# Optimization experiments

Hardware: AMD Instinct MI355X
Metric: run time of the kernel (lower is better)

Reference implementation:

```python
import jax, jax.numpy as jnp
import numpy as np
import math

D_MODEL = 1024
N_HEADS = 16
D_K = D_MODEL // N_HEADS
THETA = 0.1


def setup_inputs() -> dict:
    key = jax.random.key(0)
    ks = jax.random.split(key, 6)
    scale = np.sqrt(1.0 / D_MODEL).astype(np.float32)
    x = jax.random.normal(ks[0], (4, 2048, D_MODEL), dtype=jnp.float32)
    W_q = jax.random.normal(ks[1], (D_MODEL, D_MODEL), dtype=jnp.float32) * scale
    W_k = jax.random.normal(ks[2], (D_MODEL, D_MODEL), dtype=jnp.float32) * scale
    W_v = jax.random.normal(ks[3], (D_MODEL, D_MODEL), dtype=jnp.float32) * scale
    W_o = jax.random.normal(ks[4], (D_MODEL, D_MODEL), dtype=jnp.float32) * scale
    alpha = jnp.ones((1,), dtype=jnp.float32)
    return {"x": x, "W_q": W_q, "W_k": W_k, "W_v": W_v, "W_o": W_o, "alpha": alpha}


def reference(x, W_q, W_k, W_v, W_o, alpha):
    B, S, _ = x.shape
    Q = x @ W_q
    K = x @ W_k
    V = x @ W_v
    # non-commutative elementwise transforms
    Q = Q + THETA * jnp.sin(Q)
    K = K + THETA * jnp.cos(K)
    V = V + alpha * THETA * jnp.tanh(V)
    # split heads: [B, H, S, d_k]
    def split(t):
        return t.reshape(B, S, N_HEADS, D_K).transpose(0, 2, 1, 3)
    Qh, Kh, Vh = split(Q), split(K), split(V)
    scores = jnp.einsum('bhqd,bhkd->bhqk', Qh, Kh) / math.sqrt(D_K)
    attn = jax.nn.softmax(scores, axis=-1)
    out = jnp.einsum('bhqk,bhkd->bhqd', attn, Vh)
    out = out.transpose(0, 2, 1, 3).reshape(B, S, D_MODEL)
    return out @ W_o
```

## Files before the change

kernel.cpp:

```cpp
#include <hip/hip_runtime.h>

typedef __bf16 bf16x8 __attribute__((ext_vector_type(8)));
typedef float f32x4 __attribute__((ext_vector_type(4)));
typedef float f32x16 __attribute__((ext_vector_type(16)));

#define MFMA16(a,b,c) __builtin_amdgcn_mfma_f32_16x16x32_bf16(a,b,c,0,0,0)
#define MFMA32(a,b,c) __builtin_amdgcn_mfma_f32_32x32x16_bf16(a,b,c,0,0,0)

__device__ __forceinline__ unsigned short f2bf(float f) {
  unsigned int u = __float_as_uint(f);
  u = (u + 0x7FFFu + ((u >> 16) & 1u)) >> 16;
  return (unsigned short)u;
}

__device__ __forceinline__ void gload16(const void* g, void* l) {
  __builtin_amdgcn_global_load_lds(
      (const __attribute__((address_space(1))) void*)g,
      (__attribute__((address_space(3))) void*)l, 16, 0, 0);
}

__device__ __forceinline__ float vexp2(float x) {
  float r;
  asm("v_exp_f32 %0, %1" : "=v"(r) : "v"(x));
  return r;
}

__device__ __forceinline__ bf16x8 mk_pfrag(int hi, float p0, float p1, float p2, float p3,
                                           float p4, float p5, float p6, float p7) {
  unsigned int a0, a1, b0, b1;
  asm("v_cvt_pk_bf16_f32 %0, %1, %2" : "=v"(a0) : "v"(p0), "v"(p1));
  asm("v_cvt_pk_bf16_f32 %0, %1, %2" : "=v"(a1) : "v"(p2), "v"(p3));
  asm("v_cvt_pk_bf16_f32 %0, %1, %2" : "=v"(b0) : "v"(p4), "v"(p5));
  asm("v_cvt_pk_bf16_f32 %0, %1, %2" : "=v"(b1) : "v"(p6), "v"(p7));
  unsigned int x = __shfl_xor(hi ? a0 : b0, 32);
  unsigned int y = __shfl_xor(hi ? a1 : b1, 32);
  uint4 w;
  w.x = hi ? x : a0;
  w.y = hi ? y : a1;
  w.z = hi ? b0 : x;
  w.w = hi ? b1 : y;
  return *reinterpret_cast<bf16x8*>(&w);
}

__global__ __launch_bounds__(256) void k_convx(const float* __restrict__ x,
                                               unsigned short* __restrict__ xb) {
  int i = (blockIdx.x * 256 + threadIdx.x) * 4;
  float4 v = *reinterpret_cast<const float4*>(x + i);
  ushort4 o;
  o.x = f2bf(v.x); o.y = f2bf(v.y); o.z = f2bf(v.z); o.w = f2bf(v.w);
  *reinterpret_cast<ushort4*>(xb + i) = o;
}

__global__ __launch_bounds__(256) void k_transw(const float* __restrict__ W,
                                                unsigned short* __restrict__ WT) {
  __shared__ float t[32][33];
  int bx = blockIdx.x * 32;
  int by = blockIdx.y * 32;
  int tx = threadIdx.x & 31;
  int ty = threadIdx.x >> 5;
#pragma unroll
  for (int i = 0; i < 32; i += 8)
    t[ty + i][tx] = W[(size_t)(by + ty + i) * 1024 + bx + tx];
  __syncthreads();
#pragma unroll
  for (int i = 0; i < 32; i += 8)
    WT[(size_t)(bx + ty + i) * 1024 + by + tx] = f2bf(t[tx][ty + i]);
}

template <int EPI>
__global__ __launch_bounds__(256) void k_gemm(
    const unsigned short* __restrict__ A, const unsigned short* __restrict__ BT, int K,
    unsigned short* __restrict__ Qf, unsigned short* __restrict__ Kf,
    unsigned short* __restrict__ VT, const float* __restrict__ alphaPtr,
    float* __restrict__ Out) {
  __shared__ __align__(16) unsigned short smem[128 * 136];
  unsigned short* AsBase = smem;
  unsigned short* BsBase = smem + 128 * 32;
  const int tid = threadIdx.x;
  const int wave = tid >> 6, lane = tid & 63;
  const int l15 = lane & 15, lg = lane >> 4;
  const int wr = wave >> 1, wc = wave & 1;
  const int bm = blockIdx.x, bn = blockIdx.y;

  f32x4 acc[4][4] = {};
  const unsigned short* Ab = A + (size_t)bm * 128 * K;
  const unsigned short* Bb = BT + (size_t)bn * 128 * K;

  const int r0 = tid >> 2, q0 = (tid & 3) * 8;
  const int r1 = r0 + 64;
  char* ldsA = (char*)AsBase + wave * 1024;
  char* ldsB = (char*)BsBase + wave * 1024;

  for (int k0 = 0; k0 < K; k0 += 32) {
    gload16((const void*)(Ab + (size_t)r0 * K + k0 + q0), ldsA);
    gload16((const void*)(Ab + (size_t)r1 * K + k0 + q0), ldsA + 4096);
    gload16((const void*)(Bb + (size_t)r0 * K + k0 + q0), ldsB);
    gload16((const void*)(Bb + (size_t)r1 * K + k0 + q0), ldsB + 4096);
    __syncthreads();
    bf16x8 af[4], bfr[4];
#pragma unroll
    for (int mi = 0; mi < 4; ++mi)
      af[mi] = *reinterpret_cast<const bf16x8*>(&AsBase[(wr * 64 + mi * 16 + l15) * 32 + lg * 8]);
#pragma unroll
    for (int ni = 0; ni < 4; ++ni)
      bfr[ni] = *reinterpret_cast<const bf16x8*>(&BsBase[(wc * 64 + ni * 16 + l15) * 32 + lg * 8]);
#pragma unroll
    for (int mi = 0; mi < 4; ++mi)
#pragma unroll
      for (int ni = 0; ni < 4; ++ni)
        acc[mi][ni] = MFMA16(af[mi], bfr[ni], acc[mi][ni]);
    __syncthreads();
  }

  if (EPI == 0) {
    const float av = alphaPtr[0];
    const int t = bn >> 3;
    if (t == 2) {
#pragma unroll
      for (int mi = 0; mi < 4; ++mi) {
        int row0 = bm * 128 + wr * 64 + mi * 16 + lg * 4;
        int bb = row0 >> 11, s = row0 & 2047;
#pragma unroll
        for (int ni = 0; ni < 4; ++ni) {
          int col = (bn & 7) * 128 + wc * 64 + ni * 16 + l15;
          int hh = col >> 6, dd = col & 63;
          ushort4 pk;
#pragma unroll
          for (int r = 0; r < 4; ++r) {
            float v = acc[mi][ni][r];
            float e = __expf(2.0f * v);
            v += av * 0.1f * (1.0f - 2.0f * __builtin_amdgcn_rcpf(e + 1.0f));
            ((unsigned short*)&pk)[r] = f2bf(v);
          }
          *reinterpret_cast<ushort4*>(VT + ((size_t)(bb * 16 + hh) * 64 + dd) * 2048 + s) = pk;
        }
      }
    } else {
#pragma unroll
      for (int mi = 0; mi < 4; ++mi)
#pragma unroll
        for (int ni = 0; ni < 4; ++ni)
#pragma unroll
          for (int r = 0; r < 4; ++r) {
            int row = wr * 64 + mi * 16 + lg * 4 + r;
            int col = wc * 64 + ni * 16 + l15;
            float v = acc[mi][ni][r];
            if (t == 0) {
              v += 0.1f * __sinf(v);
              v *= 0.18033688011112042f;
            } else {
              v += 0.1f * __cosf(v);
            }
            smem[row * 136 + col] = f2bf(v);
          }
      __syncthreads();
      unsigned short* dst = (t == 0) ? Qf : Kf;
      const int c16 = tid & 15, rb = tid >> 4;
      const int ncol0 = (bn & 7) * 128;
#pragma unroll
      for (int i2 = 0; i2 < 8; ++i2) {
        int srow = rb + i2 * 16;
        uint4 val = *reinterpret_cast<const uint4*>(&smem[srow * 136 + c16 * 8]);
        *reinterpret_cast<uint4*>(dst + (size_t)(bm * 128 + srow) * 1024 + ncol0 + c16 * 8) = val;
      }
    }
  } else {
#pragma unroll
    for (int ni = 0; ni < 4; ++ni) {
      int n = bn * 128 + wc * 64 + ni * 16 + l15;
#pragma unroll
      for (int mi = 0; mi < 4; ++mi) {
        int row = bm * 128 + wr * 64 + mi * 16 + lg * 4;
#pragma unroll
        for (int r = 0; r < 4; ++r)
          Out[(size_t)(row + r) * 1024 + n] = acc[mi][ni][r];
      }
    }
  }
}

__global__ __launch_bounds__(256)
__attribute__((amdgpu_waves_per_eu(4, 4)))
void k_attn(const unsigned short* __restrict__ Qf,
            const unsigned short* __restrict__ Kf,
            const unsigned short* __restrict__ VT,
            unsigned short* __restrict__ AO) {
  __shared__ __align__(16) unsigned short smem[3 * 8192];
  const int tid = threadIdx.x;
  const int wave = tid >> 6, lane = tid & 63;
  const int l31 = lane & 31, hi = lane >> 5;
  const int f = (blockIdx.y << 4) | blockIdx.x;
  const int nf = ((f & 7) << 7) | (f >> 3);
  const int qb = nf & 15, bh = nf >> 4;
  const int b = bh >> 4, h = bh & 15;

  const unsigned short* Qb = Qf + ((size_t)b * 2048 + qb * 128 + wave * 32) * 1024 + h * 64;
  const unsigned short* Kb = Kf + (size_t)b * 2048 * 1024 + h * 64;
  const unsigned short* Vb = VT + (size_t)bh * 64 * 2048;

  bf16x8 qfr[4];
#pragma unroll
  for (int ds = 0; ds < 4; ++ds)
    qfr[ds] = *reinterpret_cast<const bf16x8*>(Qb + (size_t)l31 * 1024 + ds * 16 + hi * 8);
  asm volatile("s_waitcnt vmcnt(0)" ::: "memory");

  float lsum = 0.f;
  f32x16 o0 = {}, o1 = {};

  const int krow0 = wave * 16 + (lane >> 3);
  const int ksrcc = ((lane & 7) ^ (lane >> 3)) << 3;
  const int kxor = l31 & 7;

#pragma unroll
  for (int tt = 0; tt < 2; ++tt) {
    char* Kd = (char*)(smem + tt * 8192) + wave * 2048;
    char* Vd = (char*)(smem + tt * 8192 + 4096) + wave * 2048;
    int kn = tt * 64;
    gload16((const void*)(Kb + (size_t)(kn + krow0) * 1024 + ksrcc), Kd);
    gload16((const void*)(Kb + (size_t)(kn + krow0 + 8) * 1024 + ksrcc), Kd + 1024);
    gload16((const void*)(Vb + (size_t)krow0 * 2048 + kn + ksrcc), Vd);
    gload16((const void*)(Vb + (size_t)(krow0 + 8) * 2048 + kn + ksrcc), Vd + 1024);
  }

  for (int t = 0; t < 32; ++t) {
    const unsigned short* KsC = smem + (t % 3) * 8192;
    const unsigned short* VTC = KsC + 4096;

    if (t < 31) asm volatile("s_waitcnt vmcnt(4)" ::: "memory");
    else        asm volatile("s_waitcnt vmcnt(0)" ::: "memory");
    __builtin_amdgcn_s_barrier();
    __builtin_amdgcn_sched_barrier(0);

    if (t < 30) {
      int kn = (t + 2) * 64;
      char* Kd = (char*)(smem + ((t + 2) % 3) * 8192) + wave * 2048;
      char* Vd = (char*)(smem + ((t + 2) % 3) * 8192 + 4096) + wave * 2048;
      gload16((const void*)(Kb + (size_t)(kn + krow0) * 1024 + ksrcc), Kd);
      gload16((const void*)(Kb + (size_t)(kn + krow0 + 8) * 1024 + ksrcc), Kd + 1024);
      gload16((const void*)(Vb + (size_t)krow0 * 2048 + kn + ksrcc), Vd);
      gload16((const void*)(Vb + (size_t)(krow0 + 8) * 2048 + kn + ksrcc), Vd + 1024);
    }

    f32x16 s0 = {}, s1 = {};
    __builtin_amdgcn_s_setprio(1);
#pragma unroll
    for (int ds = 0; ds < 4; ++ds) {
      int ch = ((ds * 2 + hi) ^ kxor) * 8;
      bf16x8 kf0 = *reinterpret_cast<const bf16x8*>(&KsC[l31 * 64 + ch]);
      bf16x8 kf1 = *reinterpret_cast<const bf16x8*>(&KsC[(l31 + 32) * 64 + ch]);
      s0 = MFMA32(kf0, qfr[ds], s0);
      s1 = MFMA32(kf1, qfr[ds], s1);
    }
    __builtin_amdgcn_s_setprio(0);

    float rs0 = 0.f, rs1 = 0.f, rs2 = 0.f, rs3 = 0.f;
#pragma unroll
    for (int r = 0; r < 16; r += 4) {
      float p0 = vexp2(s0[r]);     s0[r] = p0;     rs0 += p0;
      float p1 = vexp2(s0[r + 1]); s0[r + 1] = p1; rs1 += p1;
      float p2 = vexp2(s0[r + 2]); s0[r + 2] = p2; rs2 += p2;
      float p3 = vexp2(s0[r + 3]); s0[r + 3] = p3; rs3 += p3;
    }
#pragma unroll
    for (int r = 0; r < 16; r += 4) {
      float p0 = vexp2(s1[r]);     s1[r] = p0;     rs0 += p0;
      float p1 = vexp2(s1[r + 1]); s1[r + 1] = p1; rs1 += p1;
      float p2 = vexp2(s1[r + 2]); s1[r + 2] = p2; rs2 += p2;
      float p3 = vexp2(s1[r + 3]); s1[r + 3] = p3; rs3 += p3;
    }
    lsum += (rs0 + rs1) + (rs2 + rs3);

    __builtin_amdgcn_s_setprio(1);
#pragma unroll
    for (int ks = 0; ks < 4; ++ks) {
      bf16x8 pf =
          (ks == 0) ? mk_pfrag(hi, s0[0], s0[1], s0[2], s0[3], s0[4], s0[5], s0[6], s0[7])
        : (ks == 1) ? mk_pfrag(hi, s0[8], s0[9], s0[10], s0[11], s0[12], s0[13], s0[14], s0[15])
        : (ks == 2) ? mk_pfrag(hi, s1[0], s1[1], s1[2], s1[3], s1[4], s1[5], s1[6], s1[7])
                    : mk_pfrag(hi, s1[8], s1[9], s1[10], s1[11], s1[12], s1[13], s1[14], s1[15]);
      int ch = ((ks * 2 + hi) ^ kxor) * 8;
      bf16x8 v0 = *reinterpret_cast<const bf16x8*>(&VTC[l31 * 64 + ch]);
      bf16x8 v1 = *reinterpret_cast<const bf16x8*>(&VTC[(l31 + 32) * 64 + ch]);
      o0 = MFMA32(v0, pf, o0);
      o1 = MFMA32(v1, pf, o1);
    }
    __builtin_amdgcn_s_setprio(0);
  }
  __syncthreads();

  lsum += __shfl_xor(lsum, 32);
  const float inv = 1.0f / lsum;
  unsigned short* OL = smem + wave * 2304;
#pragma unroll
  for (int r = 0; r < 16; ++r) {
    int d0 = (r & 3) + 8 * (r >> 2) + 4 * hi;
    OL[l31 * 72 + d0] = f2bf(o0[r] * inv);
    OL[l31 * 72 + 32 + d0] = f2bf(o1[r] * inv);
  }
  __syncthreads();
#pragma unroll
  for (int p = 0; p < 4; ++p) {
    int u = tid + p * 256;
    int row = u >> 3, ch = u & 7;
    uint4 val = *reinterpret_cast<const uint4*>(&smem[(row >> 5) * 2304 + (row & 31) * 72 + ch * 8]);
    *reinterpret_cast<uint4*>(AO + ((size_t)b * 2048 + qb * 128 + row) * 1024 + h * 64 + ch * 8) = val;
  }
}

extern "C" void kernel_launch(void* const* d_in, const int* in_sizes, int n_in,
                              void* d_out, int out_size, void* d_ws, size_t ws_size,
                              hipStream_t stream) {
  const float* x = (const float*)d_in[0];
  const float* Wq = (const float*)d_in[1];
  const float* Wk = (const float*)d_in[2];
  const float* Wv = (const float*)d_in[3];
  const float* Wo = (const float*)d_in[4];
  const float* alpha = (const float*)d_in[5];
  float* out = (float*)d_out;

  char* ws = (char*)d_ws;
  unsigned short* xb  = (unsigned short*)(ws);
  unsigned short* WT3 = (unsigned short*)(ws + 16777216);
  unsigned short* WoT = (unsigned short*)(ws + 23068672);
  unsigned short* Qf  = (unsigned short*)(ws + 25165824);
  unsigned short* Kf  = (unsigned short*)(ws + 41943040);
  unsigned short* VTb = (unsigned short*)(ws + 58720256);
  unsigned short* AO  = (unsigned short*)(ws + 75497472);

  k_convx<<<dim3(8192), dim3(256), 0, stream>>>(x, xb);
  k_transw<<<dim3(32, 32), dim3(256), 0, stream>>>(Wq, WT3);
  k_transw<<<dim3(32, 32), dim3(256), 0, stream>>>(Wk, WT3 + 1024 * 1024);
  k_transw<<<dim3(32, 32), dim3(256), 0, stream>>>(Wv, WT3 + 2 * 1024 * 1024);
  k_transw<<<dim3(32, 32), dim3(256), 0, stream>>>(Wo, WoT);

  k_gemm<0><<<dim3(64, 24), dim3(256), 0, stream>>>(xb, WT3, 1024, Qf, Kf, VTb, alpha, nullptr);
  k_attn<<<dim3(16, 64), dim3(256), 0, stream>>>(Qf, Kf, VTb, AO);
  k_gemm<1><<<dim3(64, 8), dim3(256), 0, stream>>>(AO, WoT, 1024, nullptr, nullptr, nullptr, nullptr, out);
}
```

Before: 226.0 us.

## Double K-step per barrier in GEMM with XOR-swizzled LDS layout and MFMA priority

```diff
diff --git a/kernel.cpp b/kernel.cpp
--- a/kernel.cpp
+++ b/kernel.cpp
@@ -74,11 +74,12 @@
     unsigned short* __restrict__ VT, const float* __restrict__ alphaPtr,
     float* __restrict__ Out) {
   __shared__ __align__(16) unsigned short smem[128 * 136];
-  unsigned short* AsBase = smem;
-  unsigned short* BsBase = smem + 128 * 32;
+  unsigned short* As = smem;
+  unsigned short* Bs = smem + 8192;
   const int tid = threadIdx.x;
   const int wave = tid >> 6, lane = tid & 63;
   const int l15 = lane & 15, lg = lane >> 4;
+  const int l7 = l15 & 7;
   const int wr = wave >> 1, wc = wave & 1;
   const int bm = blockIdx.x, bn = blockIdx.y;
 
@@ -86,29 +87,39 @@
   const unsigned short* Ab = A + (size_t)bm * 128 * K;
   const unsigned short* Bb = BT + (size_t)bn * 128 * K;
 
-  const int r0 = tid >> 2, q0 = (tid & 3) * 8;
-  const int r1 = r0 + 64;
-  char* ldsA = (char*)AsBase + wave * 1024;
-  char* ldsB = (char*)BsBase + wave * 1024;
-
-  for (int k0 = 0; k0 < K; k0 += 32) {
-    gload16((const void*)(Ab + (size_t)r0 * K + k0 + q0), ldsA);
-    gload16((const void*)(Ab + (size_t)r1 * K + k0 + q0), ldsA + 4096);
-    gload16((const void*)(Bb + (size_t)r0 * K + k0 + q0), ldsB);
-    gload16((const void*)(Bb + (size_t)r1 * K + k0 + q0), ldsB + 4096);
+  const int srow = wave * 8 + (lane >> 3);
+  const int scol = ((lane & 7) ^ (lane >> 3)) << 3;
+
+  for (int k0 = 0; k0 < K; k0 += 64) {
+#pragma unroll
+    for (int c = 0; c < 4; ++c) {
+      gload16((const void*)(Ab + (size_t)(32 * c + srow) * K + k0 + scol),
+              (char*)As + c * 4096 + wave * 1024);
+      gload16((const void*)(Bb + (size_t)(32 * c + srow) * K + k0 + scol),
+              (char*)Bs + c * 4096 + wave * 1024);
+    }
     __syncthreads();
-    bf16x8 af[4], bfr[4];
-#pragma unroll
-    for (int mi = 0; mi < 4; ++mi)
-      af[mi] = *reinterpret_cast<const bf16x8*>(&AsBase[(wr * 64 + mi * 16 + l15) * 32 + lg * 8]);
-#pragma unroll
-    for (int ni = 0; ni < 4; ++ni)
-      bfr[ni] = *reinterpret_cast<const bf16x8*>(&BsBase[(wc * 64 + ni * 16 + l15) * 32 + lg * 8]);
-#pragma unroll
-    for (int mi = 0; mi < 4; ++mi)
-#pragma unroll
-      for (int ni = 0; ni < 4; ++ni)
-        acc[mi][ni] = MFMA16(af[mi], bfr[ni], acc[mi][ni]);
+#pragma unroll
+    for (int kk = 0; kk < 2; ++kk) {
+      bf16x8 af[4], bfr[4];
+#pragma unroll
+      for (int mi = 0; mi < 4; ++mi) {
+        int R = wr * 64 + mi * 16 + l15;
+        af[mi] = *reinterpret_cast<const bf16x8*>(&As[R * 64 + (((kk * 4 + lg)) ^ l7) * 8]);
+      }
+#pragma unroll
+      for (int ni = 0; ni < 4; ++ni) {
+        int R = wc * 64 + ni * 16 + l15;
+        bfr[ni] = *reinterpret_cast<const bf16x8*>(&Bs[R * 64 + (((kk * 4 + lg)) ^ l7) * 8]);
+      }
+      __builtin_amdgcn_s_setprio(1);
+#pragma unroll
+      for (int mi = 0; mi < 4; ++mi)
+#pragma unroll
+        for (int ni = 0; ni < 4; ++ni)
+          acc[mi][ni] = MFMA16(af[mi], bfr[ni], acc[mi][ni]);
+      __builtin_amdgcn_s_setprio(0);
+    }
     __syncthreads();
   }
 
@@ -159,9 +170,9 @@
       const int ncol0 = (bn & 7) * 128;
 #pragma unroll
       for (int i2 = 0; i2 < 8; ++i2) {
-        int srow = rb + i2 * 16;
-        uint4 val = *reinterpret_cast<const uint4*>(&smem[srow * 136 + c16 * 8]);
-        *reinterpret_cast<uint4*>(dst + (size_t)(bm * 128 + srow) * 1024 + ncol0 + c16 * 8) = val;
+        int srow2 = rb + i2 * 16;
+        uint4 val = *reinterpret_cast<const uint4*>(&smem[srow2 * 136 + c16 * 8]);
+        *reinterpret_cast<uint4*>(dst + (size_t)(bm * 128 + srow2) * 1024 + ncol0 + c16 * 8) = val;
       }
     }
   } else {
```

New measurement: 219.4 us (median of 3 runs). 1.03x faster.
